# Optimization experiments

Hardware: AMD Instinct MI355X
Metric: run time of the kernel (lower is better)

## Reference

```python
import jax, jax.numpy as jnp
import numpy as np


def setup_inputs() -> dict:
    key = jax.random.key(0)
    kq, kk, kv = jax.random.split(key, 3)
    shape = (4, 8, 64, 8192)  # (b, n_heads, d, s)
    q = jax.random.normal(kq, shape, dtype=jnp.float32)
    k = jax.random.normal(kk, shape, dtype=jnp.float32)
    v = jax.random.normal(kv, shape, dtype=jnp.float32)
    return {"q": q, "k": k, "v": v}


def reference(q, k, v):
    # q, k, v: (b, n, d, s)
    q = jax.nn.softmax(q, axis=-2)        # softmax over feature dim d
    k = jax.nn.softmax(k, axis=-1)        # softmax over sequence dim s
    scale = q.shape[-2] ** (-0.5)
    q = q * scale
    # context: (b, n, d_k, d_v) = sum_s k[..., i, s] * v[..., j, s]
    context = jnp.einsum('bnis,bnjs->bnij', k, v)
    # out: (b, n, d_v, s)
    out = jnp.einsum('bnij,bnis->bnjs', context, q)
    return out
```

## Files before the change

kernel.cpp:

```cpp
#include <hip/hip_runtime.h>
#include <stdint.h>


typedef __attribute__((ext_vector_type(8))) short bf16x8;
typedef __attribute__((ext_vector_type(4))) float floatx4;

constexpr int D = 64, S = 8192, HEADS = 32;
constexpr int NC = 16;
constexpr int CHUNK = S / NC;
constexpr int NT = CHUNK / 64;

__device__ __forceinline__ short bf16_rn(float x) {
    unsigned u = __builtin_bit_cast(unsigned, x);
    return (short)((u + 0x8000u) >> 16);
}
__device__ __forceinline__ float bf16_f(short h) {
    unsigned u = ((unsigned)(unsigned short)h) << 16;
    return __builtin_bit_cast(float, u);
}
__device__ __forceinline__ void split8(const float* x, bf16x8& hi, bf16x8& lo) {
#pragma unroll
    for (int e = 0; e < 8; ++e) {
        short h = bf16_rn(x[e]);
        hi[e] = h;
        lo[e] = bf16_rn(x[e] - bf16_f(h));
    }
}

__device__ __forceinline__ void gl16(const void* g, void* l) {
    __builtin_amdgcn_global_load_lds(
        (const __attribute__((address_space(1))) unsigned int*)g,
        (__attribute__((address_space(3))) unsigned int*)l, 16, 0, 0);
}

__global__ __launch_bounds__(512, 4) void ctx_kernel(
    const float* __restrict__ K, const float* __restrict__ V,
    float* __restrict__ Cpart,
    float* __restrict__ Rpart)
{
    __shared__ char smem[2 * 2 * 16384];
    const int h = blockIdx.x, c = blockIdx.y;
    const int wave = threadIdx.x >> 6, lane = threadIdx.x & 63;
    const int m = lane & 15, quad = lane >> 4;

    const float* Kb = K + (size_t)h * D * S;
    const float* Vb = V + (size_t)h * D * S;
    const int c0 = c * CHUNK;

    const int ii = wave << 2;
    const int smat = ii >> 4;
    const int r0base = (ii & 15) << 2;
    const float* gmat = smat ? Vb : Kb;

    auto stage = [&](int buf, int t) {
        const int colf = c0 + (t << 6);
#pragma unroll
        for (int g = 0; g < 4; ++g) {
            const int r0 = r0base + (g << 2);
            const int r = r0 + (lane >> 4);
            const int su = (lane & 15) ^ (r & 7);
            const float* src = gmat + (size_t)r * S + colf + (su << 2);
            char* dst = smem + (buf << 15) + (smat << 14) + (r0 << 8);
            gl16(src, dst);
        }
    };

    const int mt = wave >> 1, nt0 = (wave & 1) << 1;
    const int rA = mt * 16 + m;
    floatx4 acc[2];
    acc[0] = (floatx4){0.f, 0.f, 0.f, 0.f};
    acc[1] = (floatx4){0.f, 0.f, 0.f, 0.f};
    float rs = 0.f;

    stage(0, 0);
    for (int t = 0; t < NT; ++t) {
        if (t + 1 < NT) {
            stage((t + 1) & 1, t + 1);
            asm volatile("s_waitcnt vmcnt(4)" ::: "memory");
        } else {
            asm volatile("s_waitcnt vmcnt(0)" ::: "memory");
        }
        asm volatile("s_barrier" ::: "memory");

        const char* kb = smem + ((t & 1) << 15);
        const char* vb = kb + 16384;
#pragma unroll
        for (int ks = 0; ks < 2; ++ks) {
            const int u0 = (ks << 3) + (quad << 1);
            float ar[8];
            const char* kr = kb + (rA << 8);
            *(float4*)&ar[0] = *(const float4*)(kr + ((u0 ^ (rA & 7)) << 4));
            *(float4*)&ar[4] = *(const float4*)(kr + (((u0 + 1) ^ (rA & 7)) << 4));
            float ex[8];
#pragma unroll
            for (int e = 0; e < 8; ++e) {
                ex[e] = __expf(ar[e]);
                rs += ex[e];
            }
            bf16x8 ah, al;
            split8(ex, ah, al);
#pragma unroll
            for (int j = 0; j < 2; ++j) {
                const int rB = (nt0 + j) * 16 + m;
                float br[8];
                const char* vr = vb + (rB << 8);
                *(float4*)&br[0] = *(const float4*)(vr + ((u0 ^ (rB & 7)) << 4));
                *(float4*)&br[4] = *(const float4*)(vr + (((u0 + 1) ^ (rB & 7)) << 4));
                bf16x8 bh, bl;
                split8(br, bh, bl);
                acc[j] = __builtin_amdgcn_mfma_f32_16x16x32_bf16(ah, bh, acc[j], 0, 0, 0);
                acc[j] = __builtin_amdgcn_mfma_f32_16x16x32_bf16(ah, bl, acc[j], 0, 0, 0);
                acc[j] = __builtin_amdgcn_mfma_f32_16x16x32_bf16(al, bh, acc[j], 0, 0, 0);
            }
        }
        asm volatile("s_barrier" ::: "memory");
    }

    rs += __shfl_xor(rs, 16, 64);
    rs += __shfl_xor(rs, 32, 64);

    const size_t pbase = (((size_t)h * NC + c) << 12);
#pragma unroll
    for (int j = 0; j < 2; ++j)
#pragma unroll
        for (int r = 0; r < 4; ++r)
            Cpart[pbase + ((size_t)(((mt * 4 + nt0 + j) * 4 + r)) << 6) + lane] =
                acc[j][r];
    if ((wave & 1) == 0 && lane < 16)
        Rpart[(((size_t)h * NC + c) << 6) + mt * 16 + lane] = rs;
}

__global__ __launch_bounds__(256) void reduce_kernel(
    const float* __restrict__ Cpart, const float* __restrict__ Rpart,
    float* __restrict__ CnT)
{
    __shared__ float invr[D];
    const int h = blockIdx.x, p = blockIdx.y, t = threadIdx.x;

    if (t < D) {
        float s = 0.f;
#pragma unroll
        for (int c = 0; c < NC; ++c)
            s += Rpart[(((size_t)h * NC + c) << 6) + t];
        invr[t] = 0.125f / s;
    }
    __syncthreads();

#pragma unroll
    for (int k = 0; k < 2; ++k) {
        const int idx = (p << 9) + (k << 8) + t;
        float s = 0.f;
#pragma unroll
        for (int c = 0; c < NC; ++c)
            s += Cpart[(((size_t)h * NC + c) << 12) + idx];
        const int tile = idx >> 8, reg = (idx >> 6) & 3, lane = idx & 63;
        const int mtl = tile >> 2, ntl = tile & 3;
        const int i = mtl * 16 + ((lane >> 4) << 2) + reg;
        const int j = ntl * 16 + (lane & 15);
        CnT[((size_t)h << 12) + j * 64 + i] = s * invr[i];
    }
}

__global__ __launch_bounds__(256) void out_kernel(
    const float* __restrict__ Q, const float* __restrict__ CnT,
    float* __restrict__ Out)
{
    const int h = blockIdx.x;
    const int wave = threadIdx.x >> 6, lane = threadIdx.x & 63;
    const int m = lane & 15, quad = lane >> 4;
    const int sbase = (blockIdx.y * 4 + wave) * 128;

    bf16x8 Ah[4][2], Al[4][2];
    const float* Cb = CnT + (size_t)h * 4096;
#pragma unroll
    for (int jt = 0; jt < 4; ++jt)
#pragma unroll
        for (int kk = 0; kk < 2; ++kk) {
            float a[8];
            const float* p = Cb + (jt * 16 + m) * 64 + kk * 32 + quad * 8;
            *(float4*)&a[0] = *(const float4*)p;
            *(float4*)&a[4] = *(const float4*)(p + 4);
            split8(a, Ah[jt][kk], Al[jt][kk]);
        }

    const float* Qb = Q + (size_t)h * D * S;
    float* Ob = Out + (size_t)h * D * S;

    for (int it = 0; it < 8; ++it) {
        const int scol = sbase + it * 16 + m;
        float e[16];
        float cs = 0.f;
#pragma unroll
        for (int kk = 0; kk < 2; ++kk)
#pragma unroll
            for (int j2 = 0; j2 < 8; ++j2) {
                const float qv = Qb[(size_t)(kk * 32 + quad * 8 + j2) * S + scol];
                const float ev = __expf(qv);
                e[kk * 8 + j2] = ev;
                cs += ev;
            }
        cs += __shfl_xor(cs, 16, 64);
        cs += __shfl_xor(cs, 32, 64);
        const float inv = 1.0f / cs;

        bf16x8 Bh[2], Bl[2];
        split8(&e[0], Bh[0], Bl[0]);
        split8(&e[8], Bh[1], Bl[1]);

#pragma unroll
        for (int jt = 0; jt < 4; ++jt) {
            floatx4 a = (floatx4){0.f, 0.f, 0.f, 0.f};
#pragma unroll
            for (int kk = 0; kk < 2; ++kk) {
                a = __builtin_amdgcn_mfma_f32_16x16x32_bf16(Ah[jt][kk], Bh[kk], a, 0, 0, 0);
                a = __builtin_amdgcn_mfma_f32_16x16x32_bf16(Ah[jt][kk], Bl[kk], a, 0, 0, 0);
                a = __builtin_amdgcn_mfma_f32_16x16x32_bf16(Al[jt][kk], Bh[kk], a, 0, 0, 0);
            }
#pragma unroll
            for (int r = 0; r < 4; ++r)
                Ob[(size_t)(jt * 16 + quad * 4 + r) * S + scol] = a[r] * inv;
        }
    }
}

extern "C" void kernel_launch(void* const* d_in, const int* in_sizes, int n_in,
                              void* d_out, int out_size, void* d_ws, size_t ws_size,
                              hipStream_t stream) {
    const float* q = (const float*)d_in[0];
    const float* k = (const float*)d_in[1];
    const float* v = (const float*)d_in[2];
    float* out = (float*)d_out;

    float* Cpart = (float*)d_ws;
    float* Rpart = Cpart + (size_t)HEADS * NC * 4096;
    float* CnT   = Rpart + (size_t)HEADS * NC * 64;

    ctx_kernel<<<dim3(HEADS, NC), 512, 0, stream>>>(k, v, Cpart, Rpart);
    reduce_kernel<<<dim3(HEADS, 8), 256, 0, stream>>>(Cpart, Rpart, CnT);
    out_kernel<<<dim3(HEADS, 16), 256, 0, stream>>>(q, CnT, out);
}
```

Baseline: 253.3 us.

## Drop LDS staging and reduce kernel; accumulate context with atomics

The context kernel now loads K and V straight from global memory into registers with a two-step software pipeline, replacing the LDS double-buffered global_load_lds staging. Partial results are combined with atomicAdd into a zeroed workspace, which removes the separate reduce kernel; normalization and the layout transpose move into the output kernel's prologue. Chunk count and output grid are doubled for more parallelism. The cost is a memset, atomic contention, and order-dependent float summation, and the uncoalesced direct global loads may raise memory traffic.

```diff
diff --git a/kernel.cpp b/kernel.cpp
--- a/kernel.cpp
+++ b/kernel.cpp
@@ -6,9 +6,9 @@
 typedef __attribute__((ext_vector_type(4))) float floatx4;
 
 constexpr int D = 64, S = 8192, HEADS = 32;
-constexpr int NC = 16;
+constexpr int NC = 32;
 constexpr int CHUNK = S / NC;
-constexpr int NT = CHUNK / 64;
+constexpr int NK = CHUNK / 32;
 
 __device__ __forceinline__ short bf16_rn(float x) {
     unsigned u = __builtin_bit_cast(unsigned, x);
@@ -27,166 +27,117 @@
     }
 }
 
-__device__ __forceinline__ void gl16(const void* g, void* l) {
-    __builtin_amdgcn_global_load_lds(
-        (const __attribute__((address_space(1))) unsigned int*)g,
-        (__attribute__((address_space(3))) unsigned int*)l, 16, 0, 0);
-}
-
-__global__ __launch_bounds__(512, 4) void ctx_kernel(
+__global__ __launch_bounds__(512, 8) void ctx_kernel(
     const float* __restrict__ K, const float* __restrict__ V,
-    float* __restrict__ Cpart,
-    float* __restrict__ Rpart)
+    float* __restrict__ C,
+    float* __restrict__ R)
 {
-    __shared__ char smem[2 * 2 * 16384];
     const int h = blockIdx.x, c = blockIdx.y;
     const int wave = threadIdx.x >> 6, lane = threadIdx.x & 63;
     const int m = lane & 15, quad = lane >> 4;
+    const int mt = wave >> 1, nt0 = (wave & 1) << 1;
 
-    const float* Kb = K + (size_t)h * D * S;
-    const float* Vb = V + (size_t)h * D * S;
-    const int c0 = c * CHUNK;
+    const float* pa = K + (size_t)h * D * S + (size_t)(mt * 16 + m) * S
+                    + c * CHUNK + quad * 8;
+    const float* pb0 = V + (size_t)h * D * S + (size_t)(nt0 * 16 + m) * S
+                     + c * CHUNK + quad * 8;
+    const float* pb1 = pb0 + (size_t)16 * S;
 
-    const int ii = wave << 2;
-    const int smat = ii >> 4;
-    const int r0base = (ii & 15) << 2;
-    const float* gmat = smat ? Vb : Kb;
-
-    auto stage = [&](int buf, int t) {
-        const int colf = c0 + (t << 6);
-#pragma unroll
-        for (int g = 0; g < 4; ++g) {
-            const int r0 = r0base + (g << 2);
-            const int r = r0 + (lane >> 4);
-            const int su = (lane & 15) ^ (r & 7);
-            const float* src = gmat + (size_t)r * S + colf + (su << 2);
-            char* dst = smem + (buf << 15) + (smat << 14) + (r0 << 8);
-            gl16(src, dst);
-        }
-    };
-
-    const int mt = wave >> 1, nt0 = (wave & 1) << 1;
-    const int rA = mt * 16 + m;
     floatx4 acc[2];
     acc[0] = (floatx4){0.f, 0.f, 0.f, 0.f};
     acc[1] = (floatx4){0.f, 0.f, 0.f, 0.f};
     float rs = 0.f;
 
-    stage(0, 0);
-    for (int t = 0; t < NT; ++t) {
-        if (t + 1 < NT) {
-            stage((t + 1) & 1, t + 1);
-            asm volatile("s_waitcnt vmcnt(4)" ::: "memory");
-        } else {
-            asm volatile("s_waitcnt vmcnt(0)" ::: "memory");
+    float ka0[8], v0a[8], v1a[8], ka1[8], v0b[8], v1b[8];
+
+    auto loadstep = [&](float* ka, float* va0, float* va1, int kk) {
+        const int off = kk * 32;
+        *(float4*)&ka[0]  = *(const float4*)(pa + off);
+        *(float4*)&ka[4]  = *(const float4*)(pa + off + 4);
+        *(float4*)&va0[0] = *(const float4*)(pb0 + off);
+        *(float4*)&va0[4] = *(const float4*)(pb0 + off + 4);
+        *(float4*)&va1[0] = *(const float4*)(pb1 + off);
+        *(float4*)&va1[4] = *(const float4*)(pb1 + off + 4);
+    };
+
+    auto compute = [&](float* ka, float* va0, float* va1) {
+        float ex[8];
+#pragma unroll
+        for (int e = 0; e < 8; ++e) {
+            ex[e] = __expf(ka[e]);
+            rs += ex[e];
         }
-        asm volatile("s_barrier" ::: "memory");
+        bf16x8 ah, al, b0h, b0l, b1h, b1l;
+        split8(ex, ah, al);
+        split8(va0, b0h, b0l);
+        split8(va1, b1h, b1l);
+        acc[0] = __builtin_amdgcn_mfma_f32_16x16x32_bf16(ah, b0h, acc[0], 0, 0, 0);
+        acc[0] = __builtin_amdgcn_mfma_f32_16x16x32_bf16(ah, b0l, acc[0], 0, 0, 0);
+        acc[0] = __builtin_amdgcn_mfma_f32_16x16x32_bf16(al, b0h, acc[0], 0, 0, 0);
+        acc[1] = __builtin_amdgcn_mfma_f32_16x16x32_bf16(ah, b1h, acc[1], 0, 0, 0);
+        acc[1] = __builtin_amdgcn_mfma_f32_16x16x32_bf16(ah, b1l, acc[1], 0, 0, 0);
+        acc[1] = __builtin_amdgcn_mfma_f32_16x16x32_bf16(al, b1h, acc[1], 0, 0, 0);
+    };
 
-        const char* kb = smem + ((t & 1) << 15);
-        const char* vb = kb + 16384;
+    loadstep(ka0, v0a, v1a, 0);
 #pragma unroll
-        for (int ks = 0; ks < 2; ++ks) {
-            const int u0 = (ks << 3) + (quad << 1);
-            float ar[8];
-            const char* kr = kb + (rA << 8);
-            *(float4*)&ar[0] = *(const float4*)(kr + ((u0 ^ (rA & 7)) << 4));
-            *(float4*)&ar[4] = *(const float4*)(kr + (((u0 + 1) ^ (rA & 7)) << 4));
-            float ex[8];
-#pragma unroll
-            for (int e = 0; e < 8; ++e) {
-                ex[e] = __expf(ar[e]);
-                rs += ex[e];
-            }
-            bf16x8 ah, al;
-            split8(ex, ah, al);
-#pragma unroll
-            for (int j = 0; j < 2; ++j) {
-                const int rB = (nt0 + j) * 16 + m;
-                float br[8];
-                const char* vr = vb + (rB << 8);
-                *(float4*)&br[0] = *(const float4*)(vr + ((u0 ^ (rB & 7)) << 4));
-                *(float4*)&br[4] = *(const float4*)(vr + (((u0 + 1) ^ (rB & 7)) << 4));
-                bf16x8 bh, bl;
-                split8(br, bh, bl);
-                acc[j] = __builtin_amdgcn_mfma_f32_16x16x32_bf16(ah, bh, acc[j], 0, 0, 0);
-                acc[j] = __builtin_amdgcn_mfma_f32_16x16x32_bf16(ah, bl, acc[j], 0, 0, 0);
-                acc[j] = __builtin_amdgcn_mfma_f32_16x16x32_bf16(al, bh, acc[j], 0, 0, 0);
-            }
-        }
-        asm volatile("s_barrier" ::: "memory");
+    for (int kk = 0; kk < NK; kk += 2) {
+        if (kk + 1 < NK) loadstep(ka1, v0b, v1b, kk + 1);
+        compute(ka0, v0a, v1a);
+        if (kk + 2 < NK) loadstep(ka0, v0a, v1a, kk + 2);
+        compute(ka1, v0b, v1b);
     }
 
     rs += __shfl_xor(rs, 16, 64);
     rs += __shfl_xor(rs, 32, 64);
 
-    const size_t pbase = (((size_t)h * NC + c) << 12);
+    float* Cb = C + ((size_t)h << 12);
 #pragma unroll
-    for (int j = 0; j < 2; ++j)
+    for (int x = 0; x < 2; ++x) {
+        const int tile = mt * 4 + nt0 + x;
 #pragma unroll
         for (int r = 0; r < 4; ++r)
-            Cpart[pbase + ((size_t)(((mt * 4 + nt0 + j) * 4 + r)) << 6) + lane] =
-                acc[j][r];
+            atomicAdd(&Cb[(tile * 4 + r) * 64 + lane], acc[x][r]);
+    }
     if ((wave & 1) == 0 && lane < 16)
-        Rpart[(((size_t)h * NC + c) << 6) + mt * 16 + lane] = rs;
+        atomicAdd(&R[(h << 6) + mt * 16 + lane], rs);
 }
 
-__global__ __launch_bounds__(256) void reduce_kernel(
-    const float* __restrict__ Cpart, const float* __restrict__ Rpart,
-    float* __restrict__ CnT)
+__global__ __launch_bounds__(256, 4) void out_kernel(
+    const float* __restrict__ Q, const float* __restrict__ C,
+    const float* __restrict__ R, float* __restrict__ Out)
 {
     __shared__ float invr[D];
-    const int h = blockIdx.x, p = blockIdx.y, t = threadIdx.x;
-
-    if (t < D) {
-        float s = 0.f;
-#pragma unroll
-        for (int c = 0; c < NC; ++c)
-            s += Rpart[(((size_t)h * NC + c) << 6) + t];
-        invr[t] = 0.125f / s;
-    }
-    __syncthreads();
-
-#pragma unroll
-    for (int k = 0; k < 2; ++k) {
-        const int idx = (p << 9) + (k << 8) + t;
-        float s = 0.f;
-#pragma unroll
-        for (int c = 0; c < NC; ++c)
-            s += Cpart[(((size_t)h * NC + c) << 12) + idx];
-        const int tile = idx >> 8, reg = (idx >> 6) & 3, lane = idx & 63;
-        const int mtl = tile >> 2, ntl = tile & 3;
-        const int i = mtl * 16 + ((lane >> 4) << 2) + reg;
-        const int j = ntl * 16 + (lane & 15);
-        CnT[((size_t)h << 12) + j * 64 + i] = s * invr[i];
-    }
-}
-
-__global__ __launch_bounds__(256) void out_kernel(
-    const float* __restrict__ Q, const float* __restrict__ CnT,
-    float* __restrict__ Out)
-{
     const int h = blockIdx.x;
     const int wave = threadIdx.x >> 6, lane = threadIdx.x & 63;
     const int m = lane & 15, quad = lane >> 4;
-    const int sbase = (blockIdx.y * 4 + wave) * 128;
+    const int sbase = (blockIdx.y * 4 + wave) * 64;
+
+    if (threadIdx.x < D)
+        invr[threadIdx.x] = 0.125f / R[(h << 6) + threadIdx.x];
+    __syncthreads();
 
     bf16x8 Ah[4][2], Al[4][2];
-    const float* Cb = CnT + (size_t)h * 4096;
+    const float* Cb = C + ((size_t)h << 12);
 #pragma unroll
     for (int jt = 0; jt < 4; ++jt)
 #pragma unroll
         for (int kk = 0; kk < 2; ++kk) {
             float a[8];
-            const float* p = Cb + (jt * 16 + m) * 64 + kk * 32 + quad * 8;
-            *(float4*)&a[0] = *(const float4*)p;
-            *(float4*)&a[4] = *(const float4*)(p + 4);
+#pragma unroll
+            for (int e = 0; e < 8; ++e) {
+                const int i = kk * 32 + quad * 8 + e;
+                const int idx = (((i >> 4) * 4 + jt) * 4 + (i & 3)) * 64
+                              + (((i & 15) >> 2) << 4) + m;
+                a[e] = Cb[idx] * invr[i];
+            }
             split8(a, Ah[jt][kk], Al[jt][kk]);
         }
 
     const float* Qb = Q + (size_t)h * D * S;
     float* Ob = Out + (size_t)h * D * S;
 
-    for (int it = 0; it < 8; ++it) {
+    for (int it = 0; it < 4; ++it) {
         const int scol = sbase + it * 16 + m;
         float e[16];
         float cs = 0.f;
@@ -231,11 +182,11 @@
     const float* v = (const float*)d_in[2];
     float* out = (float*)d_out;
 
-    float* Cpart = (float*)d_ws;
-    float* Rpart = Cpart + (size_t)HEADS * NC * 4096;
-    float* CnT   = Rpart + (size_t)HEADS * NC * 64;
+    float* C = (float*)d_ws;
+    float* R = C + (size_t)HEADS * 4096;
 
-    ctx_kernel<<<dim3(HEADS, NC), 512, 0, stream>>>(k, v, Cpart, Rpart);
-    reduce_kernel<<<dim3(HEADS, 8), 256, 0, stream>>>(Cpart, Rpart, CnT);
-    out_kernel<<<dim3(HEADS, 16), 256, 0, stream>>>(q, CnT, out);
+    hipMemsetAsync(d_ws, 0, (size_t)(HEADS * 4096 + HEADS * 64) * sizeof(float),
+                   stream);
+    ctx_kernel<<<dim3(HEADS, NC), 512, 0, stream>>>(k, v, C, R);
+    out_kernel<<<dim3(HEADS, 32), 256, 0, stream>>>(q, C, R, out);
 }
```

Result: slower. 326.7 us (+29.0%).
